# Kernel optimization log

Hardware: AMD Instinct MI355X
Metric: run time of the kernel (lower is better)

Reference implementation:

```python
import jax, jax.numpy as jnp
import numpy as np

N = 100000
E = 1600000
NFEAT = 256
NHIDDEN = 128
NCLASS = 40
NLAYERS = 8
INIT_T = 0.5


def setup_inputs() -> dict:
    key = jax.random.key(0)
    ks = jax.random.split(key, 9)
    x = jax.random.normal(ks[0], (N, NFEAT), dtype=jnp.float32)
    edge_row = jax.random.randint(ks[1], (E,), 0, N, dtype=jnp.int32)
    edge_col = jax.random.randint(ks[2], (E,), 0, N, dtype=jnp.int32)
    # small weights so the Chebyshev recurrence stays numerically tame
    edge_weight = jax.random.uniform(ks[3], (E,), dtype=jnp.float32) * (2.0 / 16.0)
    b1 = 1.0 / np.sqrt(NFEAT)
    fc1_w = jax.random.uniform(ks[4], (NFEAT, NHIDDEN), minval=-b1, maxval=b1, dtype=jnp.float32)
    fc1_b = jax.random.uniform(ks[5], (NHIDDEN,), minval=-b1, maxval=b1, dtype=jnp.float32)
    b2 = 1.0 / np.sqrt(NHIDDEN)
    fc2_w = jax.random.uniform(ks[6], (NHIDDEN, NCLASS), minval=-b2, maxval=b2, dtype=jnp.float32)
    fc2_b = jax.random.uniform(ks[7], (NCLASS,), minval=-b2, maxval=b2, dtype=jnp.float32)
    thetas = jnp.full((NLAYERS,), INIT_T, dtype=jnp.float32)
    return {"x": x, "edge_row": edge_row, "edge_col": edge_col,
            "edge_weight": edge_weight, "fc1_w": fc1_w, "fc1_b": fc1_b,
            "fc2_w": fc2_w, "fc2_b": fc2_b, "thetas": thetas}


def _spmm(edge_row, edge_col, edge_weight, t):
    # out[r] = sum_{e: row[e]=r} w[e] * t[col[e]]   (sparse L @ T)
    msgs = edge_weight[:, None] * t[edge_col]  # [E, H]
    return jax.ops.segment_sum(msgs, edge_row, num_segments=N)


def reference(x, edge_row, edge_col, edge_weight, fc1_w, fc1_b, fc2_w, fc2_b, thetas):
    # eval mode: dropout is identity
    h = jax.nn.relu(x @ fc1_w + fc1_b)  # [N, H]
    # filter 0: T_0 = h, poly = theta_0 * T_0
    t0 = h
    poly = thetas[0] * t0
    # filter 1: T_1 = L @ T_0
    t1 = _spmm(edge_row, edge_col, edge_weight, t0)
    poly = poly + thetas[1] * t1
    # remaining filters, replicating the original prevs-update order exactly
    prev0, prev1 = t0, t1
    for i in range(2, NLAYERS):
        ti = 2.0 * _spmm(edge_row, edge_col, edge_weight, prev0) - prev1
        prev1 = prev0
        prev0 = ti
        poly = poly + thetas[i] * ti
    y = poly @ fc2_w + fc2_b  # [N, nclass]
    return jax.nn.log_softmax(y, axis=1)
```

## Files before the change

### kernel.cpp

```cpp
#include <hip/hip_runtime.h>
#include <hip/hip_bf16.h>


#define NFEAT 256
#define NHID  128
#define NCLS  40
#define ELLS  48

typedef __hip_bfloat16 bf16;
typedef __attribute__((ext_vector_type(8))) short bf16x8;
typedef __attribute__((ext_vector_type(4))) float f32x4;

__device__ inline float2 load2b(const bf16* p) {
    __hip_bfloat162 v = *(const __hip_bfloat162*)p;
    return make_float2(__bfloat162float(v.x), __bfloat162float(v.y));
}
__device__ inline void store2b(bf16* p, float2 v) {
    __hip_bfloat162 o;
    o.x = __float2bfloat16(v.x);
    o.y = __float2bfloat16(v.y);
    *(__hip_bfloat162*)p = o;
}

__global__ void zero_ints(int* __restrict__ p, int n) {
    int i = blockIdx.x * blockDim.x + threadIdx.x;
    if (i < n) p[i] = 0;
}

__global__ void scatter_ell(const int* __restrict__ erow, const int* __restrict__ ecol,
                            const float* __restrict__ ew, int* __restrict__ deg,
                            int2* __restrict__ cw_ell, int E) {
    int e = blockIdx.x * blockDim.x + threadIdx.x;
    if (e < E) {
        int r = erow[e];
        int p = atomicAdd(&deg[r], 1);
        if (p < ELLS)
            cw_ell[(size_t)r * ELLS + p] = make_int2(ecol[e], __float_as_int(ew[e]));
    }
}

__global__ __launch_bounds__(256) void block_sums(
    int* __restrict__ deg, int* __restrict__ bsum, int N) {
    __shared__ int ws[4];
    int r = blockIdx.x * 256 + (int)threadIdx.x;
    int lane = threadIdx.x & 63, wv = threadIdx.x >> 6;
    int d = (r < N) ? min(deg[r], ELLS) : 0;
    if (r < N) deg[r] = d;
    int x = d;
    #pragma unroll
    for (int off = 1; off < 64; off <<= 1) x += __shfl_xor(x, off);
    if (lane == 0) ws[wv] = x;
    __syncthreads();
    if (threadIdx.x == 0) bsum[blockIdx.x] = ws[0] + ws[1] + ws[2] + ws[3];
}

__global__ __launch_bounds__(512) void scan_bsums(
    const int* __restrict__ bsum, int* __restrict__ bbase, int NB) {
    __shared__ int s[512];
    int tid = threadIdx.x;
    int v = (tid < NB) ? bsum[tid] : 0;
    s[tid] = v;
    __syncthreads();
    #pragma unroll
    for (int off = 1; off < 512; off <<= 1) {
        int t = (tid >= off) ? s[tid - off] : 0;
        __syncthreads();
        s[tid] += t;
        __syncthreads();
    }
    if (tid < NB) bbase[tid] = s[tid] - v;
}

__global__ __launch_bounds__(256) void apply_starts(
    const int* __restrict__ deg, const int* __restrict__ bbase,
    int* __restrict__ row_start, int N) {
    __shared__ int ws[4];
    int r = blockIdx.x * 256 + (int)threadIdx.x;
    int lane = threadIdx.x & 63, wv = threadIdx.x >> 6;
    int d = (r < N) ? deg[r] : 0;
    int x = d;
    #pragma unroll
    for (int off = 1; off < 64; off <<= 1) {
        int y = __shfl_up(x, off);
        if (lane >= off) x += y;
    }
    if (lane == 63) ws[wv] = x;
    __syncthreads();
    int base = bbase[blockIdx.x];
    #pragma unroll
    for (int w = 0; w < 4; ++w)
        if (w < wv) base += ws[w];
    if (r < N) row_start[r] = base + (x - d);
}

__global__ __launch_bounds__(256) void compact_copy(
    const int* __restrict__ deg, const int* __restrict__ row_start,
    const int2* __restrict__ cw_ell, int2* __restrict__ cw, int N) {
    int row = blockIdx.x * 16 + (threadIdx.x >> 4);
    if (row >= N) return;
    int l16 = threadIdx.x & 15;
    int d = deg[row];
    const int2* src = cw_ell + (size_t)row * ELLS;
    int2* dst = cw + row_start[row];
    for (int j = l16; j < d; j += 16) dst[j] = src[j];
}

__global__ void hist_kernel(const int* __restrict__ erow, int* __restrict__ deg, int E) {
    int e = blockIdx.x * blockDim.x + threadIdx.x;
    if (e < E) atomicAdd(&deg[erow[e]], 1);
}

__global__ void assign_starts_cur(int* __restrict__ deg, int* __restrict__ counter,
                                  int* __restrict__ row_start, int* __restrict__ cursor, int N) {
    int r = blockIdx.x * blockDim.x + threadIdx.x;
    int lane = threadIdx.x & 63;
    int d = (r < N) ? deg[r] : 0;
    int x = d;
    #pragma unroll
    for (int off = 1; off < 64; off <<= 1) {
        int y = __shfl_up(x, off);
        if (lane >= off) x += y;
    }
    int base = 0;
    if (lane == 63) base = atomicAdd(counter, x);
    base = __shfl(base, 63);
    int start = base + (x - d);
    if (r < N) {
        row_start[r] = start;
        cursor[r] = start;
    }
}

__global__ void scatter_compact(const int* __restrict__ erow, const int* __restrict__ ecol,
                                const float* __restrict__ ew, int* __restrict__ cursor,
                                int2* __restrict__ cw, int E) {
    int e = blockIdx.x * blockDim.x + threadIdx.x;
    if (e < E) {
        int r = erow[e];
        int p = atomicAdd(&cursor[r], 1);
        cw[p] = make_int2(ecol[e], __float_as_int(ew[e]));
    }
}

__global__ __launch_bounds__(256) void fc1_mfma(
    const float* __restrict__ x, const float* __restrict__ W,
    const float* __restrict__ bias, bf16* __restrict__ t0, int n) {
    __shared__ __align__(16) bf16 As[128 * 40];
    __shared__ __align__(16) bf16 Bs[128 * 40];

    const int tid = threadIdx.x;
    const int wave = tid >> 6;
    const int lane = tid & 63;
    const int quad = lane >> 4;
    const int lm = lane & 15;
    const int block_row = blockIdx.x * 128;

    f32x4 acc[2][8];
    #pragma unroll
    for (int s = 0; s < 2; ++s)
        #pragma unroll
        for (int t = 0; t < 8; ++t)
            acc[s][t] = (f32x4){0.f, 0.f, 0.f, 0.f};

    float bcol[8];
    #pragma unroll
    for (int t = 0; t < 8; ++t) bcol[t] = bias[t * 16 + lm];

    for (int kc = 0; kc < NFEAT; kc += 32) {
        #pragma unroll
        for (int i = 0; i < 4; ++i) {
            int idx = tid + 256 * i;
            int row = idx >> 3;
            int c4 = idx & 7;
            int grow = block_row + row;
            float4 v = make_float4(0.f, 0.f, 0.f, 0.f);
            if (grow < n) v = *(const float4*)&x[(size_t)grow * NFEAT + kc + c4 * 4];
            __hip_bfloat162 lo2, hi2;
            lo2.x = __float2bfloat16(v.x); lo2.y = __float2bfloat16(v.y);
            hi2.x = __float2bfloat16(v.z); hi2.y = __float2bfloat16(v.w);
            *(__hip_bfloat162*)&As[row * 40 + c4 * 4] = lo2;
            *(__hip_bfloat162*)&As[row * 40 + c4 * 4 + 2] = hi2;
        }
        #pragma unroll
        for (int i = 0; i < 4; ++i) {
            int idx = tid + 256 * i;
            int nn = idx & 127;
            int k4 = idx >> 7;
            const float* wp = &W[(size_t)(kc + k4 * 4) * NHID + nn];
            float v0 = wp[0];
            float v1 = wp[NHID];
            float v2 = wp[2 * NHID];
            float v3 = wp[3 * NHID];
            __hip_bfloat162 lo2, hi2;
            lo2.x = __float2bfloat16(v0); lo2.y = __float2bfloat16(v1);
            hi2.x = __float2bfloat16(v2); hi2.y = __float2bfloat16(v3);
            *(__hip_bfloat162*)&Bs[nn * 40 + k4 * 4] = lo2;
            *(__hip_bfloat162*)&Bs[nn * 40 + k4 * 4 + 2] = hi2;
        }
        __syncthreads();

        bf16x8 af0 = *(const bf16x8*)&As[(wave * 32 + lm) * 40 + quad * 8];
        bf16x8 af1 = *(const bf16x8*)&As[(wave * 32 + 16 + lm) * 40 + quad * 8];
        #pragma unroll
        for (int t = 0; t < 8; ++t) {
            bf16x8 bf = *(const bf16x8*)&Bs[(t * 16 + lm) * 40 + quad * 8];
            acc[0][t] = __builtin_amdgcn_mfma_f32_16x16x32_bf16(af0, bf, acc[0][t], 0, 0, 0);
            acc[1][t] = __builtin_amdgcn_mfma_f32_16x16x32_bf16(af1, bf, acc[1][t], 0, 0, 0);
        }
        __syncthreads();
    }

    #pragma unroll
    for (int s = 0; s < 2; ++s) {
        #pragma unroll
        for (int r = 0; r < 4; ++r) {
            int grow = block_row + wave * 32 + s * 16 + quad * 4 + r;
            if (grow >= n) continue;
            bf16* orow = t0 + (size_t)grow * NHID + lm;
            #pragma unroll
            for (int t = 0; t < 8; ++t) {
                float v = fmaxf(acc[s][t][r] + bcol[t], 0.f);
                orow[t * 16] = __float2bfloat16(v);
            }
        }
    }
}

template <bool FIRST, int PMODE>
__global__ __launch_bounds__(256) void spmm_cheb(
    const int* __restrict__ row_start, const int* __restrict__ deg,
    const int2* __restrict__ cw,
    const bf16* __restrict__ tprev, const bf16* __restrict__ tsub,
    bf16* __restrict__ tout, float* __restrict__ poly,
    const float* __restrict__ thetas, int layer, int n) {
    int lane = threadIdx.x & 63;
    int wid = (int)((blockIdx.x * (unsigned)blockDim.x + threadIdx.x) >> 6);
    if (wid >= n) return;
    int start = row_start[wid];
    int d = deg[wid];
    const int2* ep = cw + start;
    const int lo = 2 * lane;

    float2 acc = make_float2(0.f, 0.f);
    int j = 0;
    for (; j + 8 <= d; j += 8) {
        int2 e[8];
        #pragma unroll
        for (int u = 0; u < 8; ++u) e[u] = ep[j + u];
        float2 tv[8];
        #pragma unroll
        for (int u = 0; u < 8; ++u) tv[u] = load2b(tprev + (size_t)e[u].x * NHID + lo);
        #pragma unroll
        for (int u = 0; u < 8; ++u) {
            float w = __int_as_float(e[u].y);
            acc.x = fmaf(w, tv[u].x, acc.x);
            acc.y = fmaf(w, tv[u].y, acc.y);
        }
    }
    for (; j < d; ++j) {
        int2 e = ep[j];
        float w = __int_as_float(e.y);
        float2 tv = load2b(tprev + (size_t)e.x * NHID + lo);
        acc.x = fmaf(w, tv.x, acc.x);
        acc.y = fmaf(w, tv.y, acc.y);
    }

    size_t o = (size_t)wid * NHID + lo;
    float2 res, pv;
    if constexpr (FIRST) {
        res = acc;
    } else {
        pv = load2b(tsub + o);
        res = make_float2(2.f * acc.x - pv.x, 2.f * acc.y - pv.y);
    }
    if constexpr (PMODE != 3) store2b(tout + o, res);

    if constexpr (PMODE == 1) {
        float th0 = thetas[0], th12 = thetas[1] + thetas[2], th3 = thetas[3];
        float2 tpv = load2b(tprev + o);
        float2 p;
        p.x = th0 * pv.x + th12 * tpv.x + th3 * res.x;
        p.y = th0 * pv.y + th12 * tpv.y + th3 * res.y;
        *(float2*)&poly[o] = p;
    } else if constexpr (PMODE == 2 || PMODE == 3) {
        float tha = thetas[layer - 1], thb = thetas[layer];
        float2 tpv = load2b(tprev + o);
        float2 p = *(float2*)&poly[o];
        p.x += tha * tpv.x + thb * res.x;
        p.y += tha * tpv.y + thb * res.y;
        *(float2*)&poly[o] = p;
    }
}

__global__ __launch_bounds__(256) void fc2_softmax(
    const float* __restrict__ poly, const float* __restrict__ w2,
    const float* __restrict__ b2, float* __restrict__ out, int n) {
    int row = blockIdx.x * 256 + threadIdx.x;
    if (row >= n) return;

    float acc[NCLS];
    #pragma unroll
    for (int c = 0; c < NCLS; ++c) acc[c] = b2[c];

    const float* pr = poly + (size_t)row * NHID;
    #pragma unroll 1
    for (int k = 0; k < NHID; k += 4) {
        float4 p = *(const float4*)&pr[k];
        const float* wr = w2 + (size_t)k * NCLS;
        #pragma unroll
        for (int c = 0; c < NCLS; ++c) {
            acc[c] = fmaf(p.x, wr[c], acc[c]);
            acc[c] = fmaf(p.y, wr[NCLS + c], acc[c]);
            acc[c] = fmaf(p.z, wr[2 * NCLS + c], acc[c]);
            acc[c] = fmaf(p.w, wr[3 * NCLS + c], acc[c]);
        }
    }

    float m = acc[0];
    #pragma unroll
    for (int c = 1; c < NCLS; ++c) m = fmaxf(m, acc[c]);
    float s = 0.f;
    #pragma unroll
    for (int c = 0; c < NCLS; ++c) s += __expf(acc[c] - m);
    float lse = m + __logf(s);

    float* orow = out + (size_t)row * NCLS;
    #pragma unroll
    for (int c = 0; c < NCLS; c += 4) {
        float4 v = make_float4(acc[c] - lse, acc[c + 1] - lse,
                               acc[c + 2] - lse, acc[c + 3] - lse);
        *(float4*)&orow[c] = v;
    }
}

static void run_spmm_chain(const float* w2, const float* b2, const float* thetas,
                           float* out, int N,
                           const int* row_start, const int* deg, const int2* cw,
                           float* poly, bf16* tX, bf16* tY, bf16* tZ,
                           hipStream_t stream) {
    int spmm_blocks = (int)(((size_t)N * 64 + 255) / 256);
    spmm_cheb<true, 0><<<spmm_blocks, 256, 0, stream>>>(
        row_start, deg, cw, tX, (const bf16*)nullptr, tY, poly, thetas, 1, N);
    spmm_cheb<false, 1><<<spmm_blocks, 256, 0, stream>>>(
        row_start, deg, cw, tY, tX, tZ, poly, thetas, 3, N);
    spmm_cheb<false, 0><<<spmm_blocks, 256, 0, stream>>>(
        row_start, deg, cw, tZ, tY, tX, poly, thetas, 4, N);
    spmm_cheb<false, 2><<<spmm_blocks, 256, 0, stream>>>(
        row_start, deg, cw, tX, tZ, tY, poly, thetas, 5, N);
    spmm_cheb<false, 0><<<spmm_blocks, 256, 0, stream>>>(
        row_start, deg, cw, tY, tX, tZ, poly, thetas, 6, N);
    spmm_cheb<false, 3><<<spmm_blocks, 256, 0, stream>>>(
        row_start, deg, cw, tZ, tY, (bf16*)nullptr, poly, thetas, 7, N);

    fc2_softmax<<<(N + 255) / 256, 256, 0, stream>>>(poly, w2, b2, out, N);
}

extern "C" void kernel_launch(void* const* d_in, const int* in_sizes, int n_in,
                              void* d_out, int out_size, void* d_ws, size_t ws_size,
                              hipStream_t stream) {
    const float* x      = (const float*)d_in[0];
    const int*   erow   = (const int*)d_in[1];
    const int*   ecol   = (const int*)d_in[2];
    const float* ew     = (const float*)d_in[3];
    const float* w1     = (const float*)d_in[4];
    const float* b1     = (const float*)d_in[5];
    const float* w2     = (const float*)d_in[6];
    const float* b2     = (const float*)d_in[7];
    const float* thetas = (const float*)d_in[8];
    float* out = (float*)d_out;

    const int N = in_sizes[0] / NFEAT;
    const int E = in_sizes[1];
    const int NB = (N + 255) / 256;

    char* ws = (char*)d_ws;
    size_t off = 0;
    auto alloc = [&](size_t bytes) -> void* {
        off = (off + 255) & ~(size_t)255;
        void* p = ws + off;
        off += bytes;
        return p;
    };

    size_t poly_bytes = (size_t)N * NHID * 4;
    size_t ell_bytes  = (size_t)N * ELLS * 8;
    size_t tail = 3 * ((size_t)N * NHID * 2 + 256) + 4096;
    size_t need_pri = (size_t)N * 4 + (size_t)N * 4 + (size_t)(NB + 1) * 8 +
                      (size_t)E * 8 +
                      (poly_bytes > ell_bytes ? poly_bytes : ell_bytes) + tail + 8192;
    size_t need_fb  = (size_t)(N + 1) * 4 + 2 * (size_t)N * 4 + (size_t)E * 8 +
                      poly_bytes + tail + 8192;

    if (NB <= 512 && need_pri <= ws_size) {
        int*   deg       = (int*)alloc((size_t)N * 4);
        int*   row_start = (int*)alloc((size_t)N * 4);
        int*   bsum      = (int*)alloc((size_t)NB * 4);
        int*   bbase     = (int*)alloc((size_t)(NB + 1) * 4);
        int2*  cw        = (int2*)alloc((size_t)E * 8);
        float* poly      = (float*)alloc(poly_bytes > ell_bytes ? poly_bytes : ell_bytes);
        int2*  cw_ell    = (int2*)poly;
        bf16*  tX        = (bf16*)alloc((size_t)N * NHID * 2);
        bf16*  tY        = (bf16*)alloc((size_t)N * NHID * 2);
        bf16*  tZ        = (bf16*)alloc((size_t)N * NHID * 2);

        zero_ints<<<(N + 255) / 256, 256, 0, stream>>>(deg, N);
        scatter_ell<<<(E + 255) / 256, 256, 0, stream>>>(erow, ecol, ew, deg, cw_ell, E);
        block_sums<<<NB, 256, 0, stream>>>(deg, bsum, N);
        scan_bsums<<<1, 512, 0, stream>>>(bsum, bbase, NB);
        apply_starts<<<NB, 256, 0, stream>>>(deg, bbase, row_start, N);
        compact_copy<<<(N + 15) / 16, 256, 0, stream>>>(deg, row_start, cw_ell, cw, N);
        fc1_mfma<<<(N + 127) / 128, 256, 0, stream>>>(x, w1, b1, tX, N);
        run_spmm_chain(w2, b2, thetas, out, N,
                       row_start, deg, cw, poly, tX, tY, tZ, stream);
    } else {
        int*   deg       = (int*)alloc((size_t)(N + 1) * 4);
        int*   counter   = deg + N;
        int*   row_start = (int*)alloc((size_t)N * 4);
        int*   cursor    = (int*)alloc((size_t)N * 4);
        int2*  cw        = (int2*)alloc((size_t)E * 8);
        float* poly      = (float*)alloc(poly_bytes);
        bf16*  tX        = (bf16*)alloc((size_t)N * NHID * 2);
        bf16*  tY        = (bf16*)alloc((size_t)N * NHID * 2);
        bf16*  tZ        = (bf16*)alloc((size_t)N * NHID * 2);

        zero_ints<<<(N + 1 + 255) / 256, 256, 0, stream>>>(deg, N + 1);
        hist_kernel<<<(E + 255) / 256, 256, 0, stream>>>(erow, deg, E);
        assign_starts_cur<<<(N + 255) / 256, 256, 0, stream>>>(deg, counter, row_start, cursor, N);
        scatter_compact<<<(E + 255) / 256, 256, 0, stream>>>(erow, ecol, ew, cursor, cw, E);
        fc1_mfma<<<(N + 127) / 128, 256, 0, stream>>>(x, w1, b1, tX, N);
        run_spmm_chain(w2, b2, thetas, out, N,
                       row_start, deg, cw, poly, tX, tY, tZ, stream);
    }
}
```

Before: 848.4 us.

## Split SpMM chain into feature slices with four rows per wave

The Chebyshev SpMM chain is restructured to run over four 32-feature slices, each a full six-launch chain. Each wave now handles four rows with 16 lanes per row, and each lane covers two features of the slice. The aim is to shrink the gathered working set per pass (N×32 bf16, about 6.4MB) so gathers hit in cache instead of going to HBM. In exchange, the edge list is re-read four times, launch count rises to 24, and each gather is only 64 bytes per row.

```diff
diff --git a/kernel.cpp b/kernel.cpp
--- a/kernel.cpp
+++ b/kernel.cpp
@@ -6,6 +6,8 @@
 #define NHID  128
 #define NCLS  40
 #define ELLS  48
+#define NPASS 4
+#define FSL   32
 
 typedef __hip_bfloat16 bf16;
 typedef __attribute__((ext_vector_type(8))) short bf16x8;
@@ -227,19 +229,22 @@
 }
 
 template <bool FIRST, int PMODE>
-__global__ __launch_bounds__(256) void spmm_cheb(
+__global__ __launch_bounds__(256) void spmm_q(
     const int* __restrict__ row_start, const int* __restrict__ deg,
     const int2* __restrict__ cw,
     const bf16* __restrict__ tprev, const bf16* __restrict__ tsub,
     bf16* __restrict__ tout, float* __restrict__ poly,
-    const float* __restrict__ thetas, int layer, int n) {
+    const float* __restrict__ thetas, int layer, int foff, int n) {
     int lane = threadIdx.x & 63;
     int wid = (int)((blockIdx.x * (unsigned)blockDim.x + threadIdx.x) >> 6);
-    if (wid >= n) return;
-    int start = row_start[wid];
-    int d = deg[wid];
+    int sub = lane >> 4;
+    int fl = (lane & 15) * 2;
+    int r = wid * 4 + sub;
+    if (r >= n) return;
+    int start = row_start[r];
+    int d = deg[r];
     const int2* ep = cw + start;
-    const int lo = 2 * lane;
+    const bf16* tp = tprev + foff + fl;
 
     float2 acc = make_float2(0.f, 0.f);
     int j = 0;
@@ -249,7 +254,7 @@
         for (int u = 0; u < 8; ++u) e[u] = ep[j + u];
         float2 tv[8];
         #pragma unroll
-        for (int u = 0; u < 8; ++u) tv[u] = load2b(tprev + (size_t)e[u].x * NHID + lo);
+        for (int u = 0; u < 8; ++u) tv[u] = load2b(tp + (size_t)e[u].x * NHID);
         #pragma unroll
         for (int u = 0; u < 8; ++u) {
             float w = __int_as_float(e[u].y);
@@ -260,12 +265,12 @@
     for (; j < d; ++j) {
         int2 e = ep[j];
         float w = __int_as_float(e.y);
-        float2 tv = load2b(tprev + (size_t)e.x * NHID + lo);
+        float2 tv = load2b(tp + (size_t)e.x * NHID);
         acc.x = fmaf(w, tv.x, acc.x);
         acc.y = fmaf(w, tv.y, acc.y);
     }
 
-    size_t o = (size_t)wid * NHID + lo;
+    size_t o = (size_t)r * NHID + foff + fl;
     float2 res, pv;
     if constexpr (FIRST) {
         res = acc;
@@ -338,20 +343,23 @@
                            const int* row_start, const int* deg, const int2* cw,
                            float* poly, bf16* tX, bf16* tY, bf16* tZ,
                            hipStream_t stream) {
-    int spmm_blocks = (int)(((size_t)N * 64 + 255) / 256);
-    spmm_cheb<true, 0><<<spmm_blocks, 256, 0, stream>>>(
-        row_start, deg, cw, tX, (const bf16*)nullptr, tY, poly, thetas, 1, N);
-    spmm_cheb<false, 1><<<spmm_blocks, 256, 0, stream>>>(
-        row_start, deg, cw, tY, tX, tZ, poly, thetas, 3, N);
-    spmm_cheb<false, 0><<<spmm_blocks, 256, 0, stream>>>(
-        row_start, deg, cw, tZ, tY, tX, poly, thetas, 4, N);
-    spmm_cheb<false, 2><<<spmm_blocks, 256, 0, stream>>>(
-        row_start, deg, cw, tX, tZ, tY, poly, thetas, 5, N);
-    spmm_cheb<false, 0><<<spmm_blocks, 256, 0, stream>>>(
-        row_start, deg, cw, tY, tX, tZ, poly, thetas, 6, N);
-    spmm_cheb<false, 3><<<spmm_blocks, 256, 0, stream>>>(
-        row_start, deg, cw, tZ, tY, (bf16*)nullptr, poly, thetas, 7, N);
-
+    int waves = (N + 3) / 4;
+    int blocks = (waves + 3) / 4;
+    for (int p = 0; p < NPASS; ++p) {
+        int fo = p * FSL;
+        spmm_q<true, 0><<<blocks, 256, 0, stream>>>(
+            row_start, deg, cw, tX, (const bf16*)nullptr, tY, poly, thetas, 1, fo, N);
+        spmm_q<false, 1><<<blocks, 256, 0, stream>>>(
+            row_start, deg, cw, tY, tX, tZ, poly, thetas, 3, fo, N);
+        spmm_q<false, 0><<<blocks, 256, 0, stream>>>(
+            row_start, deg, cw, tZ, tY, tX, poly, thetas, 4, fo, N);
+        spmm_q<false, 2><<<blocks, 256, 0, stream>>>(
+            row_start, deg, cw, tX, tZ, tY, poly, thetas, 5, fo, N);
+        spmm_q<false, 0><<<blocks, 256, 0, stream>>>(
+            row_start, deg, cw, tY, tX, tZ, poly, thetas, 6, fo, N);
+        spmm_q<false, 3><<<blocks, 256, 0, stream>>>(
+            row_start, deg, cw, tZ, tY, (bf16*)nullptr, poly, thetas, 7, fo, N);
+    }
     fc2_softmax<<<(N + 255) / 256, 256, 0, stream>>>(poly, w2, b2, out, N);
 }
 
```

Result: slower. 1.276 ms (+50.4%).
